# Optimization experiments

Hardware: AMD Instinct MI355X
Metric: run time of the kernel (lower is better)

Reference implementation:

```python
import jax, jax.numpy as jnp
import numpy as np

N_NODES = 50000
N_EDGES = 800000
D_IN = 768
D_H = 256
N_CLASSES = 4
N_LAYERS = 3
N_GRAPHS = 64
LN_EPS = 1e-5


def setup_inputs() -> dict:
    key = jax.random.key(0)
    ks = jax.random.split(key, 12)
    x = jax.random.normal(ks[0], (N_NODES, D_IN), dtype=jnp.float32)
    edge_index = jax.random.randint(ks[1], (2, N_EDGES), 0, N_NODES)
    batch = jnp.sort(jax.random.randint(ks[2], (N_NODES,), 0, N_GRAPHS))
    s_in = 1.0 / np.sqrt(D_IN)
    s_h = 1.0 / np.sqrt(D_H)
    W_in = jax.random.normal(ks[3], (D_IN, D_H), jnp.float32) * s_in
    b_in = jnp.zeros((D_H,), jnp.float32)
    convW = jax.random.normal(ks[4], (N_LAYERS, D_H, D_H), jnp.float32) * s_h
    convB = jnp.zeros((N_LAYERS, D_H), jnp.float32)
    lnG = jnp.ones((N_LAYERS, D_H), jnp.float32)
    lnB = jnp.zeros((N_LAYERS, D_H), jnp.float32)
    clsW1 = jax.random.normal(ks[5], (D_H, D_H), jnp.float32) * s_h
    clsB1 = jnp.zeros((D_H,), jnp.float32)
    clsW2 = jax.random.normal(ks[6], (D_H, N_CLASSES), jnp.float32) * s_h
    clsB2 = jnp.zeros((N_CLASSES,), jnp.float32)
    return {"x": x, "edge_index": edge_index, "batch": batch,
            "W_in": W_in, "b_in": b_in, "convW": convW, "convB": convB,
            "lnG": lnG, "lnB": lnB, "clsW1": clsW1, "clsB1": clsB1,
            "clsW2": clsW2, "clsB2": clsB2}


def _layer_norm(h, g, b):
    mu = jnp.mean(h, axis=-1, keepdims=True)
    var = jnp.mean(jnp.square(h - mu), axis=-1, keepdims=True)
    return (h - mu) * jax.lax.rsqrt(var + LN_EPS) * g + b


def reference(x, edge_index, batch, W_in, b_in, convW, convB, lnG, lnB,
              clsW1, clsB1, clsW2, clsB2):
    N = x.shape[0]
    loops = jnp.arange(N)
    src = jnp.concatenate([edge_index[0], loops])  # self-loops (PyG GCNConv default)
    dst = jnp.concatenate([edge_index[1], loops])
    deg = jax.ops.segment_sum(jnp.ones_like(src, dtype=x.dtype), dst, num_segments=N)
    dinv = jax.lax.rsqrt(deg)  # deg >= 1 due to self-loops
    norm = dinv[src] * dinv[dst]  # symmetric GCN normalization per edge

    h = x @ W_in + b_in  # input projection -> [N, D_H]
    for i in range(N_LAYERS):
        m = h @ convW[i]  # transform then propagate
        h_new = jax.ops.segment_sum(m[src] * norm[:, None], dst, num_segments=N) + convB[i]
        h = jax.nn.relu(h_new + h)  # residual (shapes match), then ReLU
        h = _layer_norm(h, lnG[i], lnB[i])
        # dropout: identity (inference mode)

    g = jax.ops.segment_max(h, batch, num_segments=N_GRAPHS)  # global_max_pool
    z = jax.nn.relu(g @ clsW1 + clsB1)
    return z @ clsW2 + clsB2  # [N_GRAPHS, N_CLASSES]
```

## Files before the change

kernel.cpp:

```cpp
#include <hip/hip_runtime.h>
#include <hip/hip_bf16.h>
#include <math.h>

#define NNODES 50000
#define NEDGES 800000
#define DIN 768
#define DH 256
#define NCLS 4
#define NGRAPHS 64
#define SCAN_BLOCKS 196

typedef __bf16 bf16x8 __attribute__((ext_vector_type(8)));
typedef float f32x4 __attribute__((ext_vector_type(4)));

static __device__ __forceinline__ float bf2f(unsigned short u) {
    union { unsigned u32; float f; } v; v.u32 = ((unsigned)u) << 16; return v.f;
}
static __device__ __forceinline__ unsigned short f2bf(float f) {
    union { float f; unsigned u; } v; v.f = f;
    unsigned r = (v.u + 0x7fffu + ((v.u >> 16) & 1u)) >> 16;
    return (unsigned short)r;
}
static __device__ __forceinline__ void unpack8(uint4 u, float* f) {
    f[0] = bf2f((unsigned short)(u.x & 0xffff)); f[1] = bf2f((unsigned short)(u.x >> 16));
    f[2] = bf2f((unsigned short)(u.y & 0xffff)); f[3] = bf2f((unsigned short)(u.y >> 16));
    f[4] = bf2f((unsigned short)(u.z & 0xffff)); f[5] = bf2f((unsigned short)(u.z >> 16));
    f[6] = bf2f((unsigned short)(u.w & 0xffff)); f[7] = bf2f((unsigned short)(u.w >> 16));
}

__global__ void detect_dtype(const unsigned short* __restrict__ x, int* __restrict__ flag) {
    __shared__ int cnt_s;
    if (threadIdx.x == 0) cnt_s = 0;
    __syncthreads();
    int c = 0;
    for (int i = 0; i < 16; ++i) {
        float v = bf2f(x[threadIdx.x * 16 + i]);
        if (!(fabsf(v) < 1e10f)) c++;
    }
    atomicAdd(&cnt_s, c);
    __syncthreads();
    if (threadIdx.x == 0) flag[0] = (cnt_s > 32) ? 1 : 0;
}

static __device__ __forceinline__ unsigned short cload(const void* src, int i, int fp32) {
    return fp32 ? f2bf(((const float*)src)[i]) : ((const unsigned short*)src)[i];
}

__global__ void canon_small(const void* b_in, const void* convB, const void* lnG,
                            const void* lnB, const void* W1, const void* W2,
                            const void* b1, const void* b2,
                            unsigned short* __restrict__ dst, const int* __restrict__ flag) {
    int i = blockIdx.x * 256 + threadIdx.x;
    if (i >= 69380) return;
    const int fp32 = flag[0];
    int j = i;
    if (j < 256)  { dst[i] = cload(b_in, j, fp32); return; }  j -= 256;
    if (j < 768)  { dst[i] = cload(convB, j, fp32); return; } j -= 768;
    if (j < 768)  { dst[i] = cload(lnG, j, fp32); return; }   j -= 768;
    if (j < 768)  { dst[i] = cload(lnB, j, fp32); return; }   j -= 768;
    if (j < 65536){ dst[i] = cload(W1, j, fp32); return; }    j -= 65536;
    if (j < 1024) { dst[i] = cload(W2, j, fp32); return; }    j -= 1024;
    if (j < 256)  { dst[i] = cload(b1, j, fp32); return; }    j -= 256;
    dst[i] = cload(b2, j, fp32);
}

__global__ void transpose_win(const void* __restrict__ src, unsigned short* __restrict__ dst,
                              const int* __restrict__ flag) {
    int idx = blockIdx.x * 256 + threadIdx.x;
    if (idx < DIN * DH) {
        int r = idx / DH, c = idx % DH;
        dst[(size_t)c * DIN + r] = cload(src, idx, flag[0]);
    }
}
__global__ void transpose_convw(const void* __restrict__ src, unsigned short* __restrict__ dst,
                                const int* __restrict__ flag) {
    int idx = blockIdx.x * 256 + threadIdx.x;
    if (idx < 3 * DH * DH) {
        int l = idx >> 16, rc = idx & 65535;
        int r = rc >> 8, c = rc & 255;
        dst[(l << 16) + c * DH + r] = cload(src, idx, flag[0]);
    }
}

__global__ void fill_sentinel(float* out, int n) {
    int i = blockIdx.x * 256 + threadIdx.x;
    if (i < n) out[i] = 1000.0f;
}

__global__ void count_edges(const int* __restrict__ ei, int* __restrict__ cnt) {
    int e = blockIdx.x * 256 + threadIdx.x;
    if (e < NEDGES) atomicAdd(&cnt[ei[NEDGES + e]], 1);
}

__global__ void scan_local(const int* __restrict__ cnt, int* __restrict__ rowptr,
                           int* __restrict__ bsum) {
    __shared__ int tmp[256];
    int i = blockIdx.x * 256 + threadIdx.x;
    int v = (i < NNODES) ? cnt[i] : 0;
    tmp[threadIdx.x] = v;
    __syncthreads();
    for (int off = 1; off < 256; off <<= 1) {
        int a = (threadIdx.x >= off) ? tmp[threadIdx.x - off] : 0;
        __syncthreads();
        tmp[threadIdx.x] += a;
        __syncthreads();
    }
    if (i < NNODES) rowptr[i] = tmp[threadIdx.x] - v;
    if (threadIdx.x == 255) bsum[blockIdx.x] = tmp[255];
}
__global__ void scan_bsum(const int* __restrict__ bsum, int* __restrict__ boff) {
    __shared__ int tmp[256];
    int t = threadIdx.x;
    int v = (t < SCAN_BLOCKS) ? bsum[t] : 0;
    tmp[t] = v;
    __syncthreads();
    for (int off = 1; off < 256; off <<= 1) {
        int a = (t >= off) ? tmp[t - off] : 0;
        __syncthreads();
        tmp[t] += a;
        __syncthreads();
    }
    if (t < SCAN_BLOCKS) boff[t] = tmp[t] - v;
}
__global__ void scan_finish(int* __restrict__ rowptr, const int* __restrict__ boff,
                            const int* __restrict__ cnt, float* __restrict__ dinv) {
    int i = blockIdx.x * 256 + threadIdx.x;
    if (i < NNODES) {
        rowptr[i] += boff[blockIdx.x];
        dinv[i] = rsqrtf((float)(1 + cnt[i]));
    }
    if (i == 0) rowptr[NNODES] = NEDGES;
}

__global__ void fill_csr(const int* __restrict__ ei, const int* __restrict__ rowptr,
                         int* __restrict__ cursor, int* __restrict__ csrc) {
    int e = blockIdx.x * 256 + threadIdx.x;
    if (e < NEDGES) {
        int s = ei[e];
        int d = ei[NEDGES + e];
        int pos = rowptr[d] + atomicAdd(&cursor[d], 1);
        csrc[pos] = s;
    }
}

#define BM 128
#define BN 128
#define BK 32
#define LDSS 40

__global__ __launch_bounds__(256) void gemm_bf16_tn(
    const void* __restrict__ Araw, const int* __restrict__ dflag, int use_flag,
    const unsigned short* __restrict__ Bt, const unsigned short* __restrict__ bias,
    unsigned short* __restrict__ C, int M, int N, int K)
{
    __shared__ unsigned short As[BM * LDSS];
    __shared__ unsigned short Bs[BN * LDSS];
    const int a_fp32 = use_flag ? dflag[0] : 0;
    const int m0 = blockIdx.x * BM;
    const int n0 = blockIdx.y * BN;
    const int t = threadIdx.x;
    const int wave = t >> 6, lane = t & 63;
    const int quad = lane >> 4, l16 = lane & 15;
    const int wm = (wave >> 1) << 6;
    const int wn = (wave & 1) << 6;

    f32x4 acc[4][4];
#pragma unroll
    for (int i = 0; i < 4; i++)
#pragma unroll
        for (int j = 0; j < 4; j++) acc[i][j] = (f32x4){0.f, 0.f, 0.f, 0.f};

    const int lrow = t >> 2;
    const int lcg = t & 3;

    for (int k0 = 0; k0 < K; k0 += BK) {
#pragma unroll
        for (int p = 0; p < 2; ++p) {
            int row = lrow + p * 64;
            int gm = m0 + row;
            uint4 av = make_uint4(0u, 0u, 0u, 0u);
            if (gm < M) {
                if (a_fp32) {
                    const float* Af = (const float*)Araw + (size_t)gm * K + k0 + lcg * 8;
                    float4 f0 = *(const float4*)Af;
                    float4 f1 = *(const float4*)(Af + 4);
                    av.x = (unsigned)f2bf(f0.x) | ((unsigned)f2bf(f0.y) << 16);
                    av.y = (unsigned)f2bf(f0.z) | ((unsigned)f2bf(f0.w) << 16);
                    av.z = (unsigned)f2bf(f1.x) | ((unsigned)f2bf(f1.y) << 16);
                    av.w = (unsigned)f2bf(f1.z) | ((unsigned)f2bf(f1.w) << 16);
                } else {
                    av = *(const uint4*)((const unsigned short*)Araw + (size_t)gm * K + k0 + lcg * 8);
                }
            }
            *(uint4*)(&As[row * LDSS + lcg * 8]) = av;
            int gn = n0 + row;
            uint4 bv = *(const uint4*)(Bt + (size_t)gn * K + k0 + lcg * 8);
            *(uint4*)(&Bs[row * LDSS + lcg * 8]) = bv;
        }
        __syncthreads();
        bf16x8 af[4], bfv[4];
#pragma unroll
        for (int i = 0; i < 4; i++)
            af[i] = *(const bf16x8*)(&As[(wm + 16 * i + l16) * LDSS + quad * 8]);
#pragma unroll
        for (int j = 0; j < 4; j++)
            bfv[j] = *(const bf16x8*)(&Bs[(wn + 16 * j + l16) * LDSS + quad * 8]);
#pragma unroll
        for (int i = 0; i < 4; i++)
#pragma unroll
            for (int j = 0; j < 4; j++)
                acc[i][j] = __builtin_amdgcn_mfma_f32_16x16x32_bf16(af[i], bfv[j], acc[i][j], 0, 0, 0);
        __syncthreads();
    }
#pragma unroll
    for (int i = 0; i < 4; i++) {
#pragma unroll
        for (int j = 0; j < 4; j++) {
            int gc = n0 + wn + 16 * j + l16;
            float bv = bias ? bf2f(bias[gc]) : 0.f;
#pragma unroll
            for (int r = 0; r < 4; r++) {
                int gr = m0 + wm + 16 * i + quad * 4 + r;
                if (gr < M) C[(size_t)gr * N + gc] = f2bf(acc[i][j][r] + bv);
            }
        }
    }
}

__global__ __launch_bounds__(256) void aggregate_ln(
    const int* __restrict__ rowptr, const int* __restrict__ csrc,
    const float* __restrict__ dinv, const unsigned short* __restrict__ m,
    const unsigned short* __restrict__ convB,
    const unsigned short* __restrict__ lnG, const unsigned short* __restrict__ lnB,
    unsigned short* __restrict__ h)
{
    const int half = threadIdx.x >> 5;
    const int lane = threadIdx.x & 31;
    const int node = blockIdx.x * 8 + half;
    const float di = dinv[node];
    const size_t base = (size_t)node * DH + lane * 8;

    float v[8];
    unpack8(*(const uint4*)(m + base), v);
    const float selfn = di * di;
#pragma unroll
    for (int j = 0; j < 8; j++) v[j] *= selfn;

    const int k0 = rowptr[node], k1 = rowptr[node + 1];
    int k = k0;
    int sNext = (k < k1) ? csrc[k] : 0;
    while (k < k1) {
        const int s = sNext;
        const uint4 mr = *(const uint4*)(m + (size_t)s * DH + lane * 8);
        const float nrm = dinv[s] * di;
        ++k;
        if (k < k1) sNext = csrc[k];
        float mv[8];
        unpack8(mr, mv);
#pragma unroll
        for (int j = 0; j < 8; j++) v[j] += mv[j] * nrm;
    }

    float hv[8], cv[8];
    unpack8(*(const uint4*)(h + base), hv);
    unpack8(*(const uint4*)(convB + lane * 8), cv);
    float s1 = 0.f, s2 = 0.f;
#pragma unroll
    for (int j = 0; j < 8; j++) {
        v[j] = fmaxf(v[j] + cv[j] + hv[j], 0.f);
        s1 += v[j];
        s2 += v[j] * v[j];
    }
#pragma unroll
    for (int off = 16; off > 0; off >>= 1) {
        s1 += __shfl_xor(s1, off, 32);
        s2 += __shfl_xor(s2, off, 32);
    }
    const float mu = s1 * (1.f / 256.f);
    const float var = s2 * (1.f / 256.f) - mu * mu;
    const float rs = rsqrtf(var + 1e-5f);
    float gv[8], bv[8];
    unpack8(*(const uint4*)(lnG + lane * 8), gv);
    unpack8(*(const uint4*)(lnB + lane * 8), bv);
    unsigned short o[8];
#pragma unroll
    for (int j = 0; j < 8; j++) o[j] = f2bf((v[j] - mu) * rs * gv[j] + bv[j]);
    uint4 outp;
    outp.x = (unsigned)o[0] | ((unsigned)o[1] << 16);
    outp.y = (unsigned)o[2] | ((unsigned)o[3] << 16);
    outp.z = (unsigned)o[4] | ((unsigned)o[5] << 16);
    outp.w = (unsigned)o[6] | ((unsigned)o[7] << 16);
    *(uint4*)(h + base) = outp;
}

__global__ void find_bounds(const int* __restrict__ batch, int* __restrict__ s) {
    int i = blockIdx.x * 256 + threadIdx.x;
    if (i >= NNODES) return;
    int b = batch[i];
    int bp = (i == 0) ? -1 : batch[i - 1];
    for (int g = bp + 1; g <= b; ++g) s[g] = i;
    if (i == NNODES - 1)
        for (int g = b + 1; g <= NGRAPHS; ++g) s[g] = NNODES;
}

#define PSPLIT 8
__global__ __launch_bounds__(256) void pool_partial(
    const unsigned short* __restrict__ h, const int* __restrict__ s,
    float* __restrict__ pg)
{
    const int b = blockIdx.x >> 3, split = blockIdx.x & 7, f = threadIdx.x;
    const int i0 = s[b], i1 = s[b + 1];
    const int len = i1 - i0;
    const int c0 = i0 + (int)(((long)len * split) >> 3);
    const int c1 = i0 + (int)(((long)len * (split + 1)) >> 3);
    float mx = -INFINITY;
    for (int i = c0; i < c1; ++i) mx = fmaxf(mx, bf2f(h[(size_t)i * DH + f]));
    pg[(size_t)blockIdx.x * DH + f] = mx;
}
__global__ __launch_bounds__(256) void pool_reduce(const float* __restrict__ pg,
                                                   float* __restrict__ g) {
    const int b = blockIdx.x, f = threadIdx.x;
    float mx = -INFINITY;
#pragma unroll
    for (int j = 0; j < PSPLIT; ++j) mx = fmaxf(mx, pg[(size_t)(b * PSPLIT + j) * DH + f]);
    g[b * DH + f] = mx;
}

__global__ __launch_bounds__(256) void classifier(
    const float* __restrict__ g, const unsigned short* __restrict__ W1,
    const unsigned short* __restrict__ b1, const unsigned short* __restrict__ W2,
    const unsigned short* __restrict__ b2, void* __restrict__ outv,
    const int* __restrict__ flag)
{
    __shared__ float gz[DH];
    __shared__ float zz[DH];
    const int b = blockIdx.x, t = threadIdx.x;
    gz[t] = g[b * DH + t];
    __syncthreads();
    float s = bf2f(b1[t]);
    for (int k = 0; k < DH; ++k) s += gz[k] * bf2f(W1[k * DH + t]);
    zz[t] = fmaxf(s, 0.f);
    __syncthreads();
    if (t < NCLS) {
        float s2 = bf2f(b2[t]);
        for (int k = 0; k < DH; ++k) s2 += zz[k] * bf2f(W2[k * NCLS + t]);
        if (flag[0]) ((float*)outv)[b * NCLS + t] = s2;
        else ((unsigned short*)outv)[b * NCLS + t] = f2bf(s2);
    }
}

extern "C" void kernel_launch(void* const* d_in, const int* in_sizes, int n_in,
                              void* d_out, int out_size, void* d_ws, size_t ws_size,
                              hipStream_t stream)
{
    const void* x      = d_in[0];
    const int* ei      = (const int*)d_in[1];
    const int* batch   = (const int*)d_in[2];
    const void* Win    = d_in[3];
    const void* b_in   = d_in[4];
    const void* convW  = d_in[5];
    const void* convB  = d_in[6];
    const void* lnG    = d_in[7];
    const void* lnB    = d_in[8];
    const void* W1     = d_in[9];
    const void* b1     = d_in[10];
    const void* W2     = d_in[11];
    const void* b2     = d_in[12];

    char* ws = (char*)d_ws;
    unsigned short* h   = (unsigned short*)(ws + 0);
    unsigned short* m   = (unsigned short*)(ws + 25600000);
    int* csrc           = (int*)(ws + 51200000);
    int* rowptr         = (int*)(ws + 54400000);
    int* cnt            = (int*)(ws + 54600016);
    int* cursor         = (int*)(ws + 54800016);
    float* dinv         = (float*)(ws + 55000016);
    unsigned short* cw  = (unsigned short*)(ws + 55200016);
    unsigned short* WinT= (unsigned short*)(ws + 55338784);
    unsigned short* WcT = (unsigned short*)(ws + 55732000);
    float* g            = (float*)(ws + 56125216);
    float* pg           = (float*)(ws + 56190752);
    int* gb             = (int*)(ws + 56715040);
    int* bsum           = (int*)(ws + 56715312);
    int* boff           = (int*)(ws + 56716112);
    int* flag           = (int*)(ws + 56716912);
    const size_t NEED   = 56716928;
    if (ws_size < NEED) {
        fill_sentinel<<<(out_size / 2 + 255) / 256, 256, 0, stream>>>((float*)d_out, out_size / 2);
        return;
    }

    unsigned short* cBin   = cw + 0;
    unsigned short* cConvB = cw + 256;
    unsigned short* cLnG   = cw + 1024;
    unsigned short* cLnB   = cw + 1792;
    unsigned short* cW1    = cw + 2560;
    unsigned short* cW2    = cw + 68096;
    unsigned short* cB1    = cw + 69120;
    unsigned short* cB2    = cw + 69376;

    detect_dtype<<<1, 256, 0, stream>>>((const unsigned short*)x, flag);

    hipMemsetAsync(cnt, 0, 400000, stream);
    count_edges<<<(NEDGES + 255) / 256, 256, 0, stream>>>(ei, cnt);
    scan_local<<<SCAN_BLOCKS, 256, 0, stream>>>(cnt, rowptr, bsum);
    scan_bsum<<<1, 256, 0, stream>>>(bsum, boff);
    scan_finish<<<SCAN_BLOCKS, 256, 0, stream>>>(rowptr, boff, cnt, dinv);
    fill_csr<<<(NEDGES + 255) / 256, 256, 0, stream>>>(ei, rowptr, cursor, csrc);

    canon_small<<<(69380 + 255) / 256, 256, 0, stream>>>(b_in, convB, lnG, lnB, W1, W2, b1, b2, cw, flag);
    transpose_win<<<(DIN * DH + 255) / 256, 256, 0, stream>>>(Win, WinT, flag);
    transpose_convw<<<(3 * DH * DH + 255) / 256, 256, 0, stream>>>(convW, WcT, flag);

    dim3 gg((NNODES + BM - 1) / BM, DH / BN);
    gemm_bf16_tn<<<gg, 256, 0, stream>>>(x, flag, 1, WinT, cBin, h, NNODES, DH, DIN);

    for (int i = 0; i < 3; i++) {
        gemm_bf16_tn<<<gg, 256, 0, stream>>>(h, flag, 0, WcT + i * DH * DH, nullptr, m,
                                             NNODES, DH, DH);
        aggregate_ln<<<NNODES / 8, 256, 0, stream>>>(
            rowptr, csrc, dinv, m, cConvB + i * DH, cLnG + i * DH, cLnB + i * DH, h);
    }

    find_bounds<<<(NNODES + 255) / 256, 256, 0, stream>>>(batch, gb);
    pool_partial<<<NGRAPHS * PSPLIT, 256, 0, stream>>>(h, gb, pg);
    pool_reduce<<<NGRAPHS, 256, 0, stream>>>(pg, g);
    classifier<<<NGRAPHS, 256, 0, stream>>>(g, cW1, cB1, cW2, cB2, d_out, flag);
}
```

Baseline: 731.1 us.

## Double-buffer GEMM LDS tiles and software-pipeline neighbor row gathers in aggregation

The GEMM now uses two LDS buffers and prefetches the next K-tile into registers while MFMAs run on the current tile, so one barrier per iteration replaces two and global load latency is overlapped. The aggregation loop now issues the gather of the next neighbor's feature row before accumulating the current one, keeping two row loads in flight per lane. In exchange, register pressure and LDS usage rise, which may lower occupancy.

```diff
diff --git a/kernel.cpp b/kernel.cpp
--- a/kernel.cpp
+++ b/kernel.cpp
@@ -153,8 +153,8 @@
     const unsigned short* __restrict__ Bt, const unsigned short* __restrict__ bias,
     unsigned short* __restrict__ C, int M, int N, int K)
 {
-    __shared__ unsigned short As[BM * LDSS];
-    __shared__ unsigned short Bs[BN * LDSS];
+    __shared__ unsigned short As[2][BM * LDSS];
+    __shared__ unsigned short Bs[2][BN * LDSS];
     const int a_fp32 = use_flag ? dflag[0] : 0;
     const int m0 = blockIdx.x * BM;
     const int n0 = blockIdx.y * BN;
@@ -163,54 +163,88 @@
     const int quad = lane >> 4, l16 = lane & 15;
     const int wm = (wave >> 1) << 6;
     const int wn = (wave & 1) << 6;
-
-    f32x4 acc[4][4];
-#pragma unroll
-    for (int i = 0; i < 4; i++)
-#pragma unroll
-        for (int j = 0; j < 4; j++) acc[i][j] = (f32x4){0.f, 0.f, 0.f, 0.f};
-
     const int lrow = t >> 2;
     const int lcg = t & 3;
 
-    for (int k0 = 0; k0 < K; k0 += BK) {
+    f32x4 acc[4][4];
+#pragma unroll
+    for (int i = 0; i < 4; i++)
+#pragma unroll
+        for (int j = 0; j < 4; j++) acc[i][j] = (f32x4){0.f, 0.f, 0.f, 0.f};
+
+    float fA[16];
+    uint4 uA[2];
+    uint4 uB[2];
+
+    auto loadTile = [&](int k0) {
 #pragma unroll
         for (int p = 0; p < 2; ++p) {
-            int row = lrow + p * 64;
-            int gm = m0 + row;
-            uint4 av = make_uint4(0u, 0u, 0u, 0u);
-            if (gm < M) {
-                if (a_fp32) {
+            const int row = lrow + p * 64;
+            const int gm = m0 + row;
+            if (a_fp32) {
+                if (gm < M) {
                     const float* Af = (const float*)Araw + (size_t)gm * K + k0 + lcg * 8;
                     float4 f0 = *(const float4*)Af;
                     float4 f1 = *(const float4*)(Af + 4);
-                    av.x = (unsigned)f2bf(f0.x) | ((unsigned)f2bf(f0.y) << 16);
-                    av.y = (unsigned)f2bf(f0.z) | ((unsigned)f2bf(f0.w) << 16);
-                    av.z = (unsigned)f2bf(f1.x) | ((unsigned)f2bf(f1.y) << 16);
-                    av.w = (unsigned)f2bf(f1.z) | ((unsigned)f2bf(f1.w) << 16);
+                    fA[p * 8 + 0] = f0.x; fA[p * 8 + 1] = f0.y;
+                    fA[p * 8 + 2] = f0.z; fA[p * 8 + 3] = f0.w;
+                    fA[p * 8 + 4] = f1.x; fA[p * 8 + 5] = f1.y;
+                    fA[p * 8 + 6] = f1.z; fA[p * 8 + 7] = f1.w;
                 } else {
-                    av = *(const uint4*)((const unsigned short*)Araw + (size_t)gm * K + k0 + lcg * 8);
+#pragma unroll
+                    for (int j = 0; j < 8; j++) fA[p * 8 + j] = 0.f;
                 }
+            } else {
+                uA[p] = (gm < M)
+                    ? *(const uint4*)((const unsigned short*)Araw + (size_t)gm * K + k0 + lcg * 8)
+                    : make_uint4(0u, 0u, 0u, 0u);
             }
-            *(uint4*)(&As[row * LDSS + lcg * 8]) = av;
-            int gn = n0 + row;
-            uint4 bv = *(const uint4*)(Bt + (size_t)gn * K + k0 + lcg * 8);
-            *(uint4*)(&Bs[row * LDSS + lcg * 8]) = bv;
+            const int gn = n0 + row;
+            uB[p] = *(const uint4*)(Bt + (size_t)gn * K + k0 + lcg * 8);
         }
-        __syncthreads();
+    };
+    auto storeTile = [&](int buf) {
+#pragma unroll
+        for (int p = 0; p < 2; ++p) {
+            const int row = lrow + p * 64;
+            uint4 av;
+            if (a_fp32) {
+                av.x = (unsigned)f2bf(fA[p * 8 + 0]) | ((unsigned)f2bf(fA[p * 8 + 1]) << 16);
+                av.y = (unsigned)f2bf(fA[p * 8 + 2]) | ((unsigned)f2bf(fA[p * 8 + 3]) << 16);
+                av.z = (unsigned)f2bf(fA[p * 8 + 4]) | ((unsigned)f2bf(fA[p * 8 + 5]) << 16);
+                av.w = (unsigned)f2bf(fA[p * 8 + 6]) | ((unsigned)f2bf(fA[p * 8 + 7]) << 16);
+            } else {
+                av = uA[p];
+            }
+            *(uint4*)(&As[buf][row * LDSS + lcg * 8]) = av;
+            *(uint4*)(&Bs[buf][row * LDSS + lcg * 8]) = uB[p];
+        }
+    };
+
+    loadTile(0);
+    storeTile(0);
+    __syncthreads();
+    int buf = 0;
+    for (int k0 = 0; k0 < K; k0 += BK) {
+        const bool more = (k0 + BK) < K;
+        if (more) loadTile(k0 + BK);
         bf16x8 af[4], bfv[4];
 #pragma unroll
         for (int i = 0; i < 4; i++)
-            af[i] = *(const bf16x8*)(&As[(wm + 16 * i + l16) * LDSS + quad * 8]);
+            af[i] = *(const bf16x8*)(&As[buf][(wm + 16 * i + l16) * LDSS + quad * 8]);
 #pragma unroll
         for (int j = 0; j < 4; j++)
-            bfv[j] = *(const bf16x8*)(&Bs[(wn + 16 * j + l16) * LDSS + quad * 8]);
+            bfv[j] = *(const bf16x8*)(&Bs[buf][(wn + 16 * j + l16) * LDSS + quad * 8]);
 #pragma unroll
         for (int i = 0; i < 4; i++)
 #pragma unroll
             for (int j = 0; j < 4; j++)
                 acc[i][j] = __builtin_amdgcn_mfma_f32_16x16x32_bf16(af[i], bfv[j], acc[i][j], 0, 0, 0);
-        __syncthreads();
+        if (more) {
+            storeTile(buf ^ 1);
+            __syncthreads();
+            buf ^= 1;
+        }
     }
 #pragma unroll
     for (int i = 0; i < 4; i++) {
@@ -246,19 +280,29 @@
 #pragma unroll
     for (int j = 0; j < 8; j++) v[j] *= selfn;
 
-    const int k0 = rowptr[node], k1 = rowptr[node + 1];
-    int k = k0;
-    int sNext = (k < k1) ? csrc[k] : 0;
-    while (k < k1) {
-        const int s = sNext;
-        const uint4 mr = *(const uint4*)(m + (size_t)s * DH + lane * 8);
-        const float nrm = dinv[s] * di;
-        ++k;
-        if (k < k1) sNext = csrc[k];
+    const int kb = rowptr[node], ke = rowptr[node + 1];
+    int k = kb;
+    uint4 cur = make_uint4(0u, 0u, 0u, 0u);
+    float nrmC = 0.f;
+    if (k < ke) {
+        int s = csrc[k];
+        cur = *(const uint4*)(m + (size_t)s * DH + lane * 8);
+        nrmC = dinv[s] * di;
+    }
+    while (k < ke) {
+        const int kn = k + 1;
+        uint4 nxt = make_uint4(0u, 0u, 0u, 0u);
+        float nrmN = 0.f;
+        if (kn < ke) {
+            int s = csrc[kn];
+            nxt = *(const uint4*)(m + (size_t)s * DH + lane * 8);
+            nrmN = dinv[s] * di;
+        }
         float mv[8];
-        unpack8(mr, mv);
-#pragma unroll
-        for (int j = 0; j < 8; j++) v[j] += mv[j] * nrm;
+        unpack8(cur, mv);
+#pragma unroll
+        for (int j = 0; j < 8; j++) v[j] += mv[j] * nrmC;
+        cur = nxt; nrmC = nrmN; k = kn;
     }
 
     float hv[8], cv[8];
```

New measurement: 802.0 us. 1.1x slower.

## Shrink GEMM M-tile to 64 with occupancy hint; prefetch neighbor rows in aggregation

Applied to the files above, without the earlier changes.

The GEMM now uses a 64-row M tile with half the accumulators per wave and a launch-bounds occupancy hint of 4 blocks. This doubles the block count and cuts register pressure, so more waves are resident and the wave count better fits the CU count. The trade-off is less B-tile reuse per block. Separately, the aggregation loop now software-pipelines the gather, loading the next neighbor's feature row and norm while accumulating the current one, to hide gather latency.

```diff
diff --git a/kernel.cpp b/kernel.cpp
--- a/kernel.cpp
+++ b/kernel.cpp
@@ -143,12 +143,12 @@
     }
 }
 
-#define BM 128
+#define BM 64
 #define BN 128
 #define BK 32
 #define LDSS 40
 
-__global__ __launch_bounds__(256) void gemm_bf16_tn(
+__global__ __launch_bounds__(256, 4) void gemm_bf16_tn(
     const void* __restrict__ Araw, const int* __restrict__ dflag, int use_flag,
     const unsigned short* __restrict__ Bt, const unsigned short* __restrict__ bias,
     unsigned short* __restrict__ C, int M, int N, int K)
@@ -161,59 +161,58 @@
     const int t = threadIdx.x;
     const int wave = t >> 6, lane = t & 63;
     const int quad = lane >> 4, l16 = lane & 15;
-    const int wm = (wave >> 1) << 6;
+    const int wm = (wave >> 1) << 5;
     const int wn = (wave & 1) << 6;
-
-    f32x4 acc[4][4];
-#pragma unroll
-    for (int i = 0; i < 4; i++)
+    const int arow = t >> 2;
+    const int cg = t & 3;
+
+    f32x4 acc[2][4];
+#pragma unroll
+    for (int i = 0; i < 2; i++)
 #pragma unroll
         for (int j = 0; j < 4; j++) acc[i][j] = (f32x4){0.f, 0.f, 0.f, 0.f};
 
-    const int lrow = t >> 2;
-    const int lcg = t & 3;
-
     for (int k0 = 0; k0 < K; k0 += BK) {
+        const int gm = m0 + arow;
+        uint4 av = make_uint4(0u, 0u, 0u, 0u);
+        if (gm < M) {
+            if (a_fp32) {
+                const float* Af = (const float*)Araw + (size_t)gm * K + k0 + cg * 8;
+                float4 f0 = *(const float4*)Af;
+                float4 f1 = *(const float4*)(Af + 4);
+                av.x = (unsigned)f2bf(f0.x) | ((unsigned)f2bf(f0.y) << 16);
+                av.y = (unsigned)f2bf(f0.z) | ((unsigned)f2bf(f0.w) << 16);
+                av.z = (unsigned)f2bf(f1.x) | ((unsigned)f2bf(f1.y) << 16);
+                av.w = (unsigned)f2bf(f1.z) | ((unsigned)f2bf(f1.w) << 16);
+            } else {
+                av = *(const uint4*)((const unsigned short*)Araw + (size_t)gm * K + k0 + cg * 8);
+            }
+        }
+        *(uint4*)(&As[arow * LDSS + cg * 8]) = av;
 #pragma unroll
         for (int p = 0; p < 2; ++p) {
-            int row = lrow + p * 64;
-            int gm = m0 + row;
-            uint4 av = make_uint4(0u, 0u, 0u, 0u);
-            if (gm < M) {
-                if (a_fp32) {
-                    const float* Af = (const float*)Araw + (size_t)gm * K + k0 + lcg * 8;
-                    float4 f0 = *(const float4*)Af;
-                    float4 f1 = *(const float4*)(Af + 4);
-                    av.x = (unsigned)f2bf(f0.x) | ((unsigned)f2bf(f0.y) << 16);
-                    av.y = (unsigned)f2bf(f0.z) | ((unsigned)f2bf(f0.w) << 16);
-                    av.z = (unsigned)f2bf(f1.x) | ((unsigned)f2bf(f1.y) << 16);
-                    av.w = (unsigned)f2bf(f1.z) | ((unsigned)f2bf(f1.w) << 16);
-                } else {
-                    av = *(const uint4*)((const unsigned short*)Araw + (size_t)gm * K + k0 + lcg * 8);
-                }
-            }
-            *(uint4*)(&As[row * LDSS + lcg * 8]) = av;
-            int gn = n0 + row;
-            uint4 bv = *(const uint4*)(Bt + (size_t)gn * K + k0 + lcg * 8);
-            *(uint4*)(&Bs[row * LDSS + lcg * 8]) = bv;
+            const int row = arow + p * 64;
+            const int gn = n0 + row;
+            uint4 bv = *(const uint4*)(Bt + (size_t)gn * K + k0 + cg * 8);
+            *(uint4*)(&Bs[row * LDSS + cg * 8]) = bv;
         }
         __syncthreads();
-        bf16x8 af[4], bfv[4];
-#pragma unroll
-        for (int i = 0; i < 4; i++)
+        bf16x8 af[2], bfv[4];
+#pragma unroll
+        for (int i = 0; i < 2; i++)
             af[i] = *(const bf16x8*)(&As[(wm + 16 * i + l16) * LDSS + quad * 8]);
 #pragma unroll
         for (int j = 0; j < 4; j++)
             bfv[j] = *(const bf16x8*)(&Bs[(wn + 16 * j + l16) * LDSS + quad * 8]);
 #pragma unroll
-        for (int i = 0; i < 4; i++)
+        for (int i = 0; i < 2; i++)
 #pragma unroll
             for (int j = 0; j < 4; j++)
                 acc[i][j] = __builtin_amdgcn_mfma_f32_16x16x32_bf16(af[i], bfv[j], acc[i][j], 0, 0, 0);
         __syncthreads();
     }
 #pragma unroll
-    for (int i = 0; i < 4; i++) {
+    for (int i = 0; i < 2; i++) {
 #pragma unroll
         for (int j = 0; j < 4; j++) {
             int gc = n0 + wn + 16 * j + l16;
@@ -246,19 +245,29 @@
 #pragma unroll
     for (int j = 0; j < 8; j++) v[j] *= selfn;
 
-    const int k0 = rowptr[node], k1 = rowptr[node + 1];
-    int k = k0;
-    int sNext = (k < k1) ? csrc[k] : 0;
-    while (k < k1) {
-        const int s = sNext;
-        const uint4 mr = *(const uint4*)(m + (size_t)s * DH + lane * 8);
-        const float nrm = dinv[s] * di;
-        ++k;
-        if (k < k1) sNext = csrc[k];
+    const int kb = rowptr[node], ke = rowptr[node + 1];
+    int k = kb;
+    uint4 cur = make_uint4(0u, 0u, 0u, 0u);
+    float nrmC = 0.f;
+    if (k < ke) {
+        int s = csrc[k];
+        cur = *(const uint4*)(m + (size_t)s * DH + lane * 8);
+        nrmC = dinv[s] * di;
+    }
+    while (k < ke) {
+        const int kn = k + 1;
+        uint4 nxt = make_uint4(0u, 0u, 0u, 0u);
+        float nrmN = 0.f;
+        if (kn < ke) {
+            int s = csrc[kn];
+            nxt = *(const uint4*)(m + (size_t)s * DH + lane * 8);
+            nrmN = dinv[s] * di;
+        }
         float mv[8];
-        unpack8(mr, mv);
-#pragma unroll
-        for (int j = 0; j < 8; j++) v[j] += mv[j] * nrm;
+        unpack8(cur, mv);
+#pragma unroll
+        for (int j = 0; j < 8; j++) v[j] += mv[j] * nrmC;
+        cur = nxt; nrmC = nrmN; k = kn;
     }
 
     float hv[8], cv[8];
```

New measurement: 705.5 us. 3.5% less time.
